# Kernel tuning notes

Hardware: AMD Instinct MI355X
Metric: run time of the kernel (lower is better)

The kernel has to match this reference:

```python
import jax, jax.numpy as jnp
import numpy as np

# sym2 (== db2) decomposition filters from pywt
_DEC_LO = np.array([-0.12940952255126037, 0.22414386804185735,
                    0.8365163037378079, 0.48296291314453416], dtype=np.float32)
_DEC_HI = np.array([-0.48296291314453416, 0.8365163037378079,
                    -0.22414386804185735, -0.12940952255126037], dtype=np.float32)
# pytorch_wavelets flips the filters before torch's cross-correlation conv
H0R = jnp.asarray(_DEC_LO[::-1].copy())
H1R = jnp.asarray(_DEC_HI[::-1].copy())
L = 4  # filter length
LEVEL = 3


def afb1d(x):
    """One level of DWT (mode='zero'), x: (B, C, N) -> (lo, hi) each (B, C, (N+L-1)//2)."""
    N = x.shape[-1]
    out = (N + L - 1) // 2              # pywt dwt_coeff_len for mode='zero'
    p = 2 * (out - 1) - N + L           # total pad
    if p % 2 == 1:                      # odd-length signals get one extra zero at the end
        x = jnp.pad(x, ((0, 0), (0, 0), (0, 1)))
    ph = p // 2
    x = jnp.pad(x, ((0, 0), (0, 0), (ph, ph)))
    # strided windows: y[n] = sum_k h[k] * x_pad[2n + k]
    wins = [x[..., k:k + 2 * out:2][..., :out] for k in range(L)]
    lo = sum(H0R[k] * wins[k] for k in range(L))
    hi = sum(H1R[k] * wins[k] for k in range(L))
    return lo, hi


def wavelet_packet(x, level=LEVEL):
    # breadth-first, lo-first ordering == lexicographic sort of 'a'/'d' paths
    bands = [x]
    for _ in range(level):
        nxt = []
        for b in bands:
            lo, hi = afb1d(b)
            nxt.append(lo)
            nxt.append(hi)
        bands = nxt
    return bands


def setup_inputs() -> dict:
    key = jax.random.key(0)
    k1, k2, k3 = jax.random.split(key, 3)
    B, C, N, num_classes = 131072, 3, 50, 5
    total_features = 192  # 8 leaves * 3 channels * 8 samples
    x = jax.random.normal(k1, (B, C, N), dtype=jnp.float32)
    W = jax.random.normal(k2, (num_classes, total_features), dtype=jnp.float32) * 0.05
    b = jax.random.normal(k3, (num_classes,), dtype=jnp.float32) * 0.05
    return {"x": x, "W": W, "b": b}


def reference(x, W, b):
    bands = wavelet_packet(x)
    B = x.shape[0]
    feats = jnp.concatenate([band.reshape(B, -1) for band in bands], axis=1)  # (B, 192)
    return feats @ W.T + b                          # (B, 5)
```

## Files before the change

### kernel.cpp

```cpp
#include <hip/hip_runtime.h>

struct Amat { float a[64][50]; };

constexpr Amat makeA() {
    constexpr float h0[4] = { 0.48296291314453416f,  0.8365163037378079f,
                              0.22414386804185735f, -0.12940952255126037f};
    constexpr float h1[4] = {-0.12940952255126037f, -0.22414386804185735f,
                              0.8365163037378079f,  -0.48296291314453416f};
    float L1[2][26][50] = {};
    for (int band = 0; band < 2; ++band)
        for (int m = 0; m < 26; ++m)
            for (int n = 0; n < 50; ++n) {
                int k = n - 2 * m + 2;
                L1[band][m][n] = (k >= 0 && k < 4) ? (band ? h1[k] : h0[k]) : 0.0f;
            }
    float L2[4][14][50] = {};
    for (int j = 0; j < 4; ++j)
        for (int m = 0; m < 14; ++m)
            for (int n = 0; n < 50; ++n) {
                float acc = 0.0f;
                for (int k = 0; k < 4; ++k) {
                    int p = 2 * m + k - 2;
                    if (p >= 0 && p < 26)
                        acc += (j & 1 ? h1[k] : h0[k]) * L1[j >> 1][p][n];
                }
                L2[j][m][n] = acc;
            }
    Amat A = {};
    for (int j = 0; j < 8; ++j)
        for (int m = 0; m < 8; ++m)
            for (int n = 0; n < 50; ++n) {
                float acc = 0.0f;
                for (int k = 0; k < 4; ++k) {
                    int p = 2 * m + k - 2;
                    if (p >= 0 && p < 14)
                        acc += (j & 1 ? h1[k] : h0[k]) * L2[j >> 1][p][n];
                }
                A.a[j * 8 + m][n] = acc;
            }
    return A;
}

__device__ __constant__ Amat cA = makeA();

#define FMA_EL(A0,A1,A2,A3,A4, xv, ib)            \
    A0 = fmaf(sM[(ib) * 5 + 0], (xv), A0);        \
    A1 = fmaf(sM[(ib) * 5 + 1], (xv), A1);        \
    A2 = fmaf(sM[(ib) * 5 + 2], (xv), A2);        \
    A3 = fmaf(sM[(ib) * 5 + 3], (xv), A3);        \
    A4 = fmaf(sM[(ib) * 5 + 4], (xv), A4);

__global__ __launch_bounds__(256) void dwt_fused(const float* __restrict__ x,
                                                 const float* __restrict__ W,
                                                 const float* __restrict__ bias,
                                                 float* __restrict__ out) {
    __shared__ float sW[960];
    __shared__ float sM[752];
    const int tid = threadIdx.x;
    const size_t r0 = (size_t)blockIdx.x * 512 + 2 * (size_t)tid;
    const float4* __restrict__ xr = (const float4*)(x + r0 * 150);

    float4 q0 = xr[0], q1 = xr[1], q2 = xr[2], q3 = xr[3];
    float4 q4 = xr[4], q5 = xr[5], q6 = xr[6], q7 = xr[7];

    #pragma unroll
    for (int t = 0; t < 4; ++t) {
        const int idx = tid + t * 256;
        if (idx < 960) sW[idx] = W[idx];
    }
    __syncthreads();

    if (tid < 150) {
        const int c = tid / 50, n = tid - c * 50;
        float m0 = 0.f, m1 = 0.f, m2 = 0.f, m3 = 0.f, m4 = 0.f;
        #pragma unroll 16
        for (int f = 0; f < 64; ++f) {
            const float av = cA.a[f][n];
            const int wj = (f >> 3) * 24 + c * 8 + (f & 7);
            m0 = fmaf(sW[0 * 192 + wj], av, m0);
            m1 = fmaf(sW[1 * 192 + wj], av, m1);
            m2 = fmaf(sW[2 * 192 + wj], av, m2);
            m3 = fmaf(sW[3 * 192 + wj], av, m3);
            m4 = fmaf(sW[4 * 192 + wj], av, m4);
        }
        float* dst = &sM[tid * 5];
        dst[0] = m0; dst[1] = m1; dst[2] = m2; dst[3] = m3; dst[4] = m4;
    }
    __syncthreads();

    float a0 = 0.f, a1 = 0.f, a2 = 0.f, a3 = 0.f, a4 = 0.f;
    float b0 = 0.f, b1 = 0.f, b2 = 0.f, b3 = 0.f, b4 = 0.f;

    {
        const float4 qs[8] = {q0, q1, q2, q3, q4, q5, q6, q7};
        #pragma unroll
        for (int j = 0; j < 8; ++j) {
            const float4 q = qs[j];
            FMA_EL(a0,a1,a2,a3,a4, q.x, 4*j + 0)
            FMA_EL(a0,a1,a2,a3,a4, q.y, 4*j + 1)
            FMA_EL(a0,a1,a2,a3,a4, q.z, 4*j + 2)
            FMA_EL(a0,a1,a2,a3,a4, q.w, 4*j + 3)
        }
    }
    #pragma unroll 8
    for (int j = 8; j < 37; ++j) {
        const float4 q = xr[j];
        FMA_EL(a0,a1,a2,a3,a4, q.x, 4*j + 0)
        FMA_EL(a0,a1,a2,a3,a4, q.y, 4*j + 1)
        FMA_EL(a0,a1,a2,a3,a4, q.z, 4*j + 2)
        FMA_EL(a0,a1,a2,a3,a4, q.w, 4*j + 3)
    }
    {
        const float4 q = xr[37];
        FMA_EL(a0,a1,a2,a3,a4, q.x, 148)
        FMA_EL(a0,a1,a2,a3,a4, q.y, 149)
        FMA_EL(b0,b1,b2,b3,b4, q.z, 0)
        FMA_EL(b0,b1,b2,b3,b4, q.w, 1)
    }
    #pragma unroll 8
    for (int j = 38; j < 75; ++j) {
        const float4 q = xr[j];
        const int ib = 4*j - 150;
        FMA_EL(b0,b1,b2,b3,b4, q.x, ib + 0)
        FMA_EL(b0,b1,b2,b3,b4, q.y, ib + 1)
        FMA_EL(b0,b1,b2,b3,b4, q.z, ib + 2)
        FMA_EL(b0,b1,b2,b3,b4, q.w, ib + 3)
    }

    const float c0 = bias[0], c1 = bias[1], c2 = bias[2], c3 = bias[3], c4 = bias[4];
    float* o = out + r0 * 5;
    o[0] = a0 + c0;  o[1] = a1 + c1;  o[2] = a2 + c2;  o[3] = a3 + c3;  o[4] = a4 + c4;
    o[5] = b0 + c0;  o[6] = b1 + c1;  o[7] = b2 + c2;  o[8] = b3 + c3;  o[9] = b4 + c4;
}

extern "C" void kernel_launch(void* const* d_in, const int* in_sizes, int n_in,
                              void* d_out, int out_size, void* d_ws, size_t ws_size,
                              hipStream_t stream) {
    const float* x    = (const float*)d_in[0];
    const float* W    = (const float*)d_in[1];
    const float* bias = (const float*)d_in[2];
    float*       out  = (float*)d_out;

    const int B = in_sizes[0] / 150;
    dwt_fused<<<B / 512, 256, 0, stream>>>(x, W, bias, out);
}
```

Before: 27.60 us.

## Split M precompute into separate kernel and stream x through LDS with async loads

```diff
diff --git a/kernel.cpp b/kernel.cpp
--- a/kernel.cpp
+++ b/kernel.cpp
@@ -43,26 +43,11 @@
 
 __device__ __constant__ Amat cA = makeA();
 
-#define FMA_EL(A0,A1,A2,A3,A4, xv, ib)            \
-    A0 = fmaf(sM[(ib) * 5 + 0], (xv), A0);        \
-    A1 = fmaf(sM[(ib) * 5 + 1], (xv), A1);        \
-    A2 = fmaf(sM[(ib) * 5 + 2], (xv), A2);        \
-    A3 = fmaf(sM[(ib) * 5 + 3], (xv), A3);        \
-    A4 = fmaf(sM[(ib) * 5 + 4], (xv), A4);
-
-__global__ __launch_bounds__(256) void dwt_fused(const float* __restrict__ x,
-                                                 const float* __restrict__ W,
-                                                 const float* __restrict__ bias,
-                                                 float* __restrict__ out) {
+__global__ __launch_bounds__(256) void build_M(const float* __restrict__ W,
+                                               const float* __restrict__ bias,
+                                               float* __restrict__ Mg) {
     __shared__ float sW[960];
-    __shared__ float sM[752];
     const int tid = threadIdx.x;
-    const size_t r0 = (size_t)blockIdx.x * 512 + 2 * (size_t)tid;
-    const float4* __restrict__ xr = (const float4*)(x + r0 * 150);
-
-    float4 q0 = xr[0], q1 = xr[1], q2 = xr[2], q3 = xr[3];
-    float4 q4 = xr[4], q5 = xr[5], q6 = xr[6], q7 = xr[7];
-
     #pragma unroll
     for (int t = 0; t < 4; ++t) {
         const int idx = tid + t * 256;
@@ -83,54 +68,104 @@
             m3 = fmaf(sW[3 * 192 + wj], av, m3);
             m4 = fmaf(sW[4 * 192 + wj], av, m4);
         }
-        float* dst = &sM[tid * 5];
+        const int slot = (tid < 120) ? ((tid / 40) * 200 + (tid % 40) * 5)
+                                     : (600 + (tid - 110) * 5);
+        float* dst = &Mg[slot];
         dst[0] = m0; dst[1] = m1; dst[2] = m2; dst[3] = m3; dst[4] = m4;
+    } else if (tid < 160) {
+        float* dst = &Mg[600 + (tid - 150) * 5];
+        dst[0] = 0.f; dst[1] = 0.f; dst[2] = 0.f; dst[3] = 0.f; dst[4] = 0.f;
+    } else if (tid < 165) {
+        Mg[800 + (tid - 160)] = bias[tid - 160];
     }
-    __syncthreads();
+}
+
+#define RPB  256
+#define QDW  40
+#define QBUF (RPB * QDW)
+
+typedef const __attribute__((address_space(1))) void* gptr_t;
+typedef       __attribute__((address_space(3))) void* lptr_t;
+
+__global__ __launch_bounds__(256) void dwt_gemv(const float* __restrict__ x,
+                                                const float* __restrict__ Mg,
+                                                float* __restrict__ out) {
+    extern __shared__ float sX[];
+    const int tid  = threadIdx.x;
+    const int lane = tid & 63;
+    const int w    = tid >> 6;
+    const size_t row0 = (size_t)blockIdx.x * RPB;
+
+    auto issue = [&](int buf, int qq) {
+        const int fbase = (qq < 3) ? qq * 40 : 110;
+        #pragma unroll
+        for (int s = 0; s < 10; ++s) {
+            const int dw = (w * 10 + s) * 256 + lane * 4;
+            const int t  = dw / QDW;
+            const int d  = dw - t * QDW;
+            const int vv = ((t ^ (t >> 3)) & 7) << 2;
+            const int l  = (d < 32) ? (d ^ vv) : (d ^ (vv & 4));
+            const int src = ((int)row0 + t) * 150 + fbase + l;
+            __builtin_amdgcn_global_load_lds((gptr_t)(x + src),
+                                             (lptr_t)(sX + buf * QBUF + dw),
+                                             16, 0, 0);
+        }
+    };
+
+    const int t_self = tid;
+    const int v_self = ((t_self ^ (t_self >> 3)) & 7) << 2;
 
     float a0 = 0.f, a1 = 0.f, a2 = 0.f, a3 = 0.f, a4 = 0.f;
-    float b0 = 0.f, b1 = 0.f, b2 = 0.f, b3 = 0.f, b4 = 0.f;
 
-    {
-        const float4 qs[8] = {q0, q1, q2, q3, q4, q5, q6, q7};
+    issue(0, 0);
+
+    #pragma unroll
+    for (int q = 0; q < 4; ++q) {
+        if (q < 3) {
+            __builtin_amdgcn_sched_barrier(0);
+            issue((q + 1) & 1, q + 1);
+            asm volatile("s_waitcnt vmcnt(10)" ::: "memory");
+        } else {
+            asm volatile("s_waitcnt vmcnt(0)" ::: "memory");
+        }
+        __builtin_amdgcn_sched_barrier(0);
+
+        const float* __restrict__ xr = sX + (q & 1) * QBUF + t_self * QDW;
         #pragma unroll
-        for (int j = 0; j < 8; ++j) {
-            const float4 q = qs[j];
-            FMA_EL(a0,a1,a2,a3,a4, q.x, 4*j + 0)
-            FMA_EL(a0,a1,a2,a3,a4, q.y, 4*j + 1)
-            FMA_EL(a0,a1,a2,a3,a4, q.z, 4*j + 2)
-            FMA_EL(a0,a1,a2,a3,a4, q.w, 4*j + 3)
+        for (int j = 0; j < 10; ++j) {
+            const int d  = 4 * j;
+            const int ds = (d < 32) ? (d ^ v_self) : (d ^ (v_self & 4));
+            const float4 xv = *(const float4*)&xr[ds];
+            const float* m = Mg + q * 200 + d * 5;
+            a0 = fmaf(m[ 0], xv.x, a0);
+            a1 = fmaf(m[ 1], xv.x, a1);
+            a2 = fmaf(m[ 2], xv.x, a2);
+            a3 = fmaf(m[ 3], xv.x, a3);
+            a4 = fmaf(m[ 4], xv.x, a4);
+            a0 = fmaf(m[ 5], xv.y, a0);
+            a1 = fmaf(m[ 6], xv.y, a1);
+            a2 = fmaf(m[ 7], xv.y, a2);
+            a3 = fmaf(m[ 8], xv.y, a3);
+            a4 = fmaf(m[ 9], xv.y, a4);
+            a0 = fmaf(m[10], xv.z, a0);
+            a1 = fmaf(m[11], xv.z, a1);
+            a2 = fmaf(m[12], xv.z, a2);
+            a3 = fmaf(m[13], xv.z, a3);
+            a4 = fmaf(m[14], xv.z, a4);
+            a0 = fmaf(m[15], xv.w, a0);
+            a1 = fmaf(m[16], xv.w, a1);
+            a2 = fmaf(m[17], xv.w, a2);
+            a3 = fmaf(m[18], xv.w, a3);
+            a4 = fmaf(m[19], xv.w, a4);
         }
     }
-    #pragma unroll 8
-    for (int j = 8; j < 37; ++j) {
-        const float4 q = xr[j];
-        FMA_EL(a0,a1,a2,a3,a4, q.x, 4*j + 0)
-        FMA_EL(a0,a1,a2,a3,a4, q.y, 4*j + 1)
-        FMA_EL(a0,a1,a2,a3,a4, q.z, 4*j + 2)
-        FMA_EL(a0,a1,a2,a3,a4, q.w, 4*j + 3)
-    }
-    {
-        const float4 q = xr[37];
-        FMA_EL(a0,a1,a2,a3,a4, q.x, 148)
-        FMA_EL(a0,a1,a2,a3,a4, q.y, 149)
-        FMA_EL(b0,b1,b2,b3,b4, q.z, 0)
-        FMA_EL(b0,b1,b2,b3,b4, q.w, 1)
-    }
-    #pragma unroll 8
-    for (int j = 38; j < 75; ++j) {
-        const float4 q = xr[j];
-        const int ib = 4*j - 150;
-        FMA_EL(b0,b1,b2,b3,b4, q.x, ib + 0)
-        FMA_EL(b0,b1,b2,b3,b4, q.y, ib + 1)
-        FMA_EL(b0,b1,b2,b3,b4, q.z, ib + 2)
-        FMA_EL(b0,b1,b2,b3,b4, q.w, ib + 3)
-    }
 
-    const float c0 = bias[0], c1 = bias[1], c2 = bias[2], c3 = bias[3], c4 = bias[4];
-    float* o = out + r0 * 5;
-    o[0] = a0 + c0;  o[1] = a1 + c1;  o[2] = a2 + c2;  o[3] = a3 + c3;  o[4] = a4 + c4;
-    o[5] = b0 + c0;  o[6] = b1 + c1;  o[7] = b2 + c2;  o[8] = b3 + c3;  o[9] = b4 + c4;
+    float* o = out + (row0 + tid) * 5;
+    o[0] = a0 + Mg[800];
+    o[1] = a1 + Mg[801];
+    o[2] = a2 + Mg[802];
+    o[3] = a3 + Mg[803];
+    o[4] = a4 + Mg[804];
 }
 
 extern "C" void kernel_launch(void* const* d_in, const int* in_sizes, int n_in,
@@ -140,7 +175,17 @@
     const float* W    = (const float*)d_in[1];
     const float* bias = (const float*)d_in[2];
     float*       out  = (float*)d_out;
+    float*       Mg   = (float*)d_ws;
 
-    const int B = in_sizes[0] / 150;
-    dwt_fused<<<B / 512, 256, 0, stream>>>(x, W, bias, out);
+    build_M<<<1, 256, 0, stream>>>(W, bias, Mg);
+
+    const int B    = in_sizes[0] / 150;
+    const int grid = B / RPB;
+    const size_t smem = 2 * QBUF * sizeof(float);
+
+    (void)hipFuncSetAttribute((const void*)dwt_gemv,
+                              hipFuncAttributeMaxDynamicSharedMemorySize,
+                              (int)smem);
+
+    dwt_gemv<<<grid, 256, smem, stream>>>(x, Mg, out);
 }
```

New measurement: 32.31 us. +17.0%, slower.
